# Performance work log

Measured on AMD Instinct MI355X. Metric: run time of the kernel, lower is better.

Reference implementation:

```python
import jax, jax.numpy as jnp
import numpy as np

B, T, C, H = 16, 2048, 1024, 64

def setup_inputs() -> dict:
    key = jax.random.key(0)
    kx, kq, kk, kv = jax.random.split(key, 4)
    x = jax.random.normal(kx, (B, T, C), dtype=jnp.float32)
    Wq = jax.random.normal(kq, (C, H), dtype=jnp.float32) * (C ** -0.5)
    Wk = jax.random.normal(kk, (C, H), dtype=jnp.float32) * (C ** -0.5)
    Wv = jax.random.normal(kv, (C, H), dtype=jnp.float32) * (C ** -0.5)
    return {"x": x, "Wq": Wq, "Wk": Wk, "Wv": Wv}

def reference(x, Wq, Wk, Wv):
    # q,k,v: [B,T,H]
    q = jnp.einsum('btc,ch->bth', x, Wq)
    k = jnp.einsum('btc,ch->bth', x, Wk)
    v = jnp.einsum('btc,ch->bth', x, Wv)
    scale = k.shape[-1] ** -0.5
    # scores: [B,T,T], causal mask then softmax (dropout=0 -> identity)
    w = jnp.einsum('bth,bsh->bts', q, k) * scale
    causal = jnp.tril(jnp.ones((x.shape[1], x.shape[1]), dtype=bool))
    w = jnp.where(causal[None, :, :], w, -jnp.inf)
    w = jax.nn.softmax(w, axis=-1)
    out = jnp.einsum('bts,bsh->bth', w, v)
    return out
```

## Files before the change

### kernel.cpp

```cpp
#include <hip/hip_runtime.h>


#define B_ 16
#define T_ 2048
#define C_ 1024
#define H_ 64
#define QK_ELEMS (B_ * T_ * H_)

typedef float  f32x4  __attribute__((ext_vector_type(4)));
typedef __bf16 bf16x8 __attribute__((ext_vector_type(8)));
typedef __bf16 bf16x4 __attribute__((ext_vector_type(4)));

__device__ __forceinline__ void glds16(const void* g, void* l) {
    __builtin_amdgcn_global_load_lds(
        (const __attribute__((address_space(1))) void*)g,
        (__attribute__((address_space(3))) void*)l, 16, 0, 0);
}

__global__ __launch_bounds__(256) void wt_kernel(const float* __restrict__ Wq,
                                                 const float* __restrict__ Wk,
                                                 const float* __restrict__ Wv,
                                                 __bf16* __restrict__ Wt) {
    __shared__ float tl[64][65];
    const int mat = blockIdx.x >> 4;
    const int c0  = (blockIdx.x & 15) * 64;
    const float* W = (mat == 0) ? Wq : (mat == 1) ? Wk : Wv;
    const int t  = threadIdx.x;
    const int r4 = t >> 6;
    const int cc = t & 63;
#pragma unroll
    for (int i = 0; i < 16; i++) {
        const int c = r4 + i * 4;
        tl[c][cc] = W[(size_t)(c0 + c) * H_ + cc];
    }
    __syncthreads();
#pragma unroll
    for (int i = 0; i < 16; i++) {
        const int h = r4 + i * 4;
        const int cc2 = ((((cc >> 3) ^ (h & 7)) << 3) | (cc & 7));
        Wt[(size_t)mat * 65536 + (size_t)h * C_ + c0 + cc2] = (__bf16)tl[cc][h];
    }
}

__global__ __launch_bounds__(256) void qkv_kernel(const float* __restrict__ x,
                                                  const __bf16* __restrict__ Wt,
                                                  __bf16* __restrict__ Qw,
                                                  __bf16* __restrict__ Kw,
                                                  __bf16* __restrict__ Vtw) {
    __shared__ __align__(16) __bf16 Alds[2][64 * 72];
    __shared__ __align__(16) __bf16 Blds[2][192 * 64];

    const int tid  = threadIdx.x;
    const int w    = tid >> 6;
    const int lane = tid & 63;
    const int quad = lane >> 4;
    const int l15  = lane & 15;
    const int wm   = (w & 1) * 32;
    const int wn   = (w >> 1) * 96;
    const int m0   = blockIdx.x * 64;

    f32x4 acc[12];
#pragma unroll
    for (int i = 0; i < 12; i++) acc[i] = (f32x4){0.f, 0.f, 0.f, 0.f};

    const int ar = tid >> 3;
    const int ac = (tid & 7) * 8;
    const float* xA = x + (size_t)(m0 + ar) * C_ + ac;
    const __bf16* bsrc = Wt + (size_t)(w * 48 + (lane >> 3)) * C_ + (lane & 7) * 8;

    float4 a0, a1, a2, a3;
    auto loadA = [&](int k0) {
        a0 = *(const float4*)(xA + k0);
        a1 = *(const float4*)(xA + k0 + 4);
        a2 = *(const float4*)(xA + k0 + 32 * C_);
        a3 = *(const float4*)(xA + k0 + 32 * C_ + 4);
    };
    auto storeA = [&](int buf) {
        bf16x8 v0, v1;
        v0[0]=(__bf16)a0.x; v0[1]=(__bf16)a0.y; v0[2]=(__bf16)a0.z; v0[3]=(__bf16)a0.w;
        v0[4]=(__bf16)a1.x; v0[5]=(__bf16)a1.y; v0[6]=(__bf16)a1.z; v0[7]=(__bf16)a1.w;
        v1[0]=(__bf16)a2.x; v1[1]=(__bf16)a2.y; v1[2]=(__bf16)a2.z; v1[3]=(__bf16)a2.w;
        v1[4]=(__bf16)a3.x; v1[5]=(__bf16)a3.y; v1[6]=(__bf16)a3.z; v1[7]=(__bf16)a3.w;
        *(bf16x8*)&Alds[buf][ar * 72 + ac]        = v0;
        *(bf16x8*)&Alds[buf][(ar + 32) * 72 + ac] = v1;
    };
    auto asyncB = [&](int k0, int buf) {
        __bf16* dst = &Blds[buf][(w * 48) * 64];
        const __bf16* src = bsrc + k0;
#pragma unroll
        for (int i = 0; i < 6; i++)
            glds16(src + (size_t)i * 8 * C_, dst + i * 8 * 64);
    };

    asyncB(0, 0); loadA(0); storeA(0);

    for (int k = 0; k < 16; k++) {
        __syncthreads();
        const int kn = k + 1;
        if (kn < 16) { asyncB(kn * 64, kn & 1); loadA(kn * 64); }
        const int buf = k & 1;
#pragma unroll
        for (int kh = 0; kh < 2; kh++) {
            bf16x8 af0 = *(const bf16x8*)&Alds[buf][(wm + l15) * 72 + kh * 32 + quad * 8];
            bf16x8 af1 = *(const bf16x8*)&Alds[buf][(wm + 16 + l15) * 72 + kh * 32 + quad * 8];
            const int ch8 = ((((kh << 2) + quad) ^ (l15 & 7)) << 3);
#pragma unroll
            for (int nt = 0; nt < 6; nt++) {
                bf16x8 bfr = *(const bf16x8*)&Blds[buf][(wn + nt * 16 + l15) * 64 + ch8];
                acc[nt]     = __builtin_amdgcn_mfma_f32_16x16x32_bf16(af0, bfr, acc[nt], 0, 0, 0);
                acc[6 + nt] = __builtin_amdgcn_mfma_f32_16x16x32_bf16(af1, bfr, acc[6 + nt], 0, 0, 0);
            }
        }
        if (kn < 16) storeA(kn & 1);
    }

#pragma unroll
    for (int mt = 0; mt < 2; mt++) {
        const int row0 = m0 + wm + mt * 16 + quad * 4;
#pragma unroll
        for (int nt = 0; nt < 6; nt++) {
            const int col = wn + nt * 16 + l15;
            const f32x4 a = acc[mt * 6 + nt];
            if (wn + nt * 16 < 64) {
#pragma unroll
                for (int r = 0; r < 4; r++)
                    Qw[(size_t)(row0 + r) * H_ + col] = (__bf16)a[r];
            } else if (wn + nt * 16 < 128) {
#pragma unroll
                for (int r = 0; r < 4; r++)
                    Kw[(size_t)(row0 + r) * H_ + col - 64] = (__bf16)a[r];
            }
        }
    }
    __bf16* Vt_l = &Alds[0][0];
    if (w >= 2) {
#pragma unroll
        for (int mt = 0; mt < 2; mt++) {
            const int t0 = wm + mt * 16 + quad * 4;
#pragma unroll
            for (int nt = 2; nt < 6; nt++) {
                const int h = (nt - 2) * 16 + l15;
                const f32x4 a = acc[mt * 6 + nt];
                bf16x4 pv;
                pv[0]=(__bf16)a[0]; pv[1]=(__bf16)a[1]; pv[2]=(__bf16)a[2]; pv[3]=(__bf16)a[3];
                *(bf16x4*)&Vt_l[h * 72 + t0] = pv;
            }
        }
    }
    __syncthreads();
    if (w >= 2) {
        const int bb   = m0 >> 11;
        const int tblk = m0 & 2047;
#pragma unroll
        for (int i = 0; i < 4; i++) {
            const int hh = (w - 2) * 32 + i * 8 + (lane >> 3);
            const int tt = (lane & 7) * 8;
            *(bf16x8*)(Vtw + (((size_t)(bb * H_ + hh)) << 11) + tblk + tt) =
                *(const bf16x8*)&Vt_l[hh * 72 + tt];
        }
    }
}

#define SCALE_LOG2E 0.18033688011112042f

__global__ __launch_bounds__(256) void attn_kernel(const __bf16* __restrict__ Qw,
                                                   const __bf16* __restrict__ Kw,
                                                   const __bf16* __restrict__ Vtw,
                                                   float* __restrict__ Opart,
                                                   float* __restrict__ Lpart) {
    __shared__ __align__(16) __bf16 Klds[2][64 * 72];
    __shared__ __align__(16) __bf16 Vlds[2][64 * 72];
    __shared__ __align__(16) __bf16 Plds[4][16 * 72];

    const int tid  = threadIdx.x;
    const int w    = tid >> 6;
    const int lane = tid & 63;
    const int quad = lane >> 4;
    const int l15  = lane & 15;

    const int b   = blockIdx.x & 15;
    const int cid = 79 - (blockIdx.x >> 4);
    int qi, ci;
    if (cid < 8)       { qi = cid;                  ci = 0; }
    else if (cid < 24) { qi = 8 + ((cid - 8) >> 1); ci = (cid - 8) & 1; }
    else if (cid < 48) { const int u = cid - 24; const int d = u / 3;
                         qi = 16 + d;               ci = u - d * 3; }
    else               { qi = 24 + ((cid - 48) >> 2); ci = (cid - 48) & 3; }
    const int j0 = ci * 8;
    const int j1 = (j0 + 8 < qi + 1) ? j0 + 8 : qi + 1;
    const int nj = j1 - j0;
    const int tq0 = qi * 64;
    const size_t bT = (size_t)b * T_;

    const __bf16* qp = Qw + (bT + tq0 + w * 16 + l15) * H_ + quad * 8;
    const bf16x8 qf0 = *(const bf16x8*)qp;
    const bf16x8 qf1 = *(const bf16x8*)(qp + 32);

    float l_acc = 0.f;
    f32x4 accO[4];
#pragma unroll
    for (int nt = 0; nt < 4; nt++) accO[nt] = (f32x4){0.f, 0.f, 0.f, 0.f};

    const int sr = tid >> 3;
    const int sc = (tid & 7) * 8;
    const __bf16* Kbase = Kw + (bT + sr) * H_ + sc;
    const __bf16* Vbase = Vtw + (((size_t)(b * H_ + sr)) << 11) + sc;

    bf16x8 kr0, kr1, vr0, vr1;
    auto loadTile = [&](int ts0) {
        kr0 = *(const bf16x8*)(Kbase + (size_t)ts0 * H_);
        kr1 = *(const bf16x8*)(Kbase + (size_t)(ts0 + 32) * H_);
        vr0 = *(const bf16x8*)(Vbase + ts0);
        vr1 = *(const bf16x8*)(Vbase + ts0 + ((size_t)32 << 11));
    };
    auto storeTile = [&](int buf) {
        *(bf16x8*)&Klds[buf][sr * 72 + sc]        = kr0;
        *(bf16x8*)&Klds[buf][(sr + 32) * 72 + sc] = kr1;
        *(bf16x8*)&Vlds[buf][sr * 72 + sc]        = vr0;
        *(bf16x8*)&Vlds[buf][(sr + 32) * 72 + sc] = vr1;
    };

    loadTile(j0 * 64); storeTile(0);

    for (int jj = 0; jj < nj; jj++) {
        const int j = j0 + jj;
        __syncthreads();
        if (jj + 1 < nj) loadTile((j + 1) * 64);
        const int buf = jj & 1;

        f32x4 s[4];
#pragma unroll
        for (int nt = 0; nt < 4; nt++) {
            const __bf16* kb = &Klds[buf][(nt * 16 + l15) * 72];
            bf16x8 kf0 = *(const bf16x8*)(kb + quad * 8);
            bf16x8 kf1 = *(const bf16x8*)(kb + 32 + quad * 8);
            f32x4 z = (f32x4){0.f, 0.f, 0.f, 0.f};
            z     = __builtin_amdgcn_mfma_f32_16x16x32_bf16(kf0, qf0, z, 0, 0, 0);
            s[nt] = __builtin_amdgcn_mfma_f32_16x16x32_bf16(kf1, qf1, z, 0, 0, 0);
        }

        float p[4][4];
        if (j == qi) {
            const int ts0 = j * 64;
            const int qg  = tq0 + w * 16 + l15;
#pragma unroll
            for (int nt = 0; nt < 4; nt++)
#pragma unroll
                for (int r = 0; r < 4; r++) {
                    const int key = ts0 + nt * 16 + quad * 4 + r;
                    float e = exp2f(__builtin_fmaf(s[nt][r], SCALE_LOG2E, -8.0f));
                    e = (key > qg) ? 0.f : e;
                    p[nt][r] = e;
                    l_acc += e;
                }
        } else {
#pragma unroll
            for (int nt = 0; nt < 4; nt++)
#pragma unroll
                for (int r = 0; r < 4; r++) {
                    float e = exp2f(__builtin_fmaf(s[nt][r], SCALE_LOG2E, -8.0f));
                    p[nt][r] = e;
                    l_acc += e;
                }
        }

        __bf16* pw = &Plds[w][l15 * 72 + quad * 4];
#pragma unroll
        for (int nt = 0; nt < 4; nt++) {
            bf16x4 pv;
            pv[0]=(__bf16)p[nt][0]; pv[1]=(__bf16)p[nt][1];
            pv[2]=(__bf16)p[nt][2]; pv[3]=(__bf16)p[nt][3];
            *(bf16x4*)(pw + nt * 16) = pv;
        }
        __asm__ __volatile__("s_waitcnt lgkmcnt(0)" ::: "memory");

        const __bf16* pr = &Plds[w][l15 * 72];
        bf16x8 pf0 = *(const bf16x8*)(pr + quad * 8);
        bf16x8 pf1 = *(const bf16x8*)(pr + 32 + quad * 8);
#pragma unroll
        for (int nt = 0; nt < 4; nt++) {
            const __bf16* vb = &Vlds[buf][(nt * 16 + l15) * 72];
            bf16x8 vf0 = *(const bf16x8*)(vb + quad * 8);
            bf16x8 vf1 = *(const bf16x8*)(vb + 32 + quad * 8);
            accO[nt] = __builtin_amdgcn_mfma_f32_16x16x32_bf16(pf0, vf0, accO[nt], 0, 0, 0);
            accO[nt] = __builtin_amdgcn_mfma_f32_16x16x32_bf16(pf1, vf1, accO[nt], 0, 0, 0);
        }
        if (jj + 1 < nj) storeTile((jj + 1) & 1);
    }

    l_acc += __shfl_xor(l_acc, 16);
    l_acc += __shfl_xor(l_acc, 32);

    const int slot = (((b << 5) + qi) << 2) + ci;
    float* Op = Opart + (size_t)slot * 4096;
#pragma unroll
    for (int nt = 0; nt < 4; nt++)
#pragma unroll
        for (int r = 0; r < 4; r++)
            Op[(w * 16 + quad * 4 + r) * 64 + nt * 16 + l15] = accO[nt][r];
    if (quad == 0) Lpart[slot * 64 + w * 16 + l15] = l_acc;
}

__global__ __launch_bounds__(256) void reduce_kernel(const float* __restrict__ Opart,
                                                     const float* __restrict__ Lpart,
                                                     float* __restrict__ out) {
    const int b  = blockIdx.x & 15;
    const int qi = blockIdx.x >> 4;
    const int nc = (qi >> 3) + 1;
    const int tid = threadIdx.x;
    const int q  = tid >> 2;
    const int hc = (tid & 3) * 16;
    const int sbase = ((b << 5) + qi) << 2;

    f32x4 s[4];
#pragma unroll
    for (int i = 0; i < 4; i++) s[i] = (f32x4){0.f, 0.f, 0.f, 0.f};
    float l = 0.f;
    for (int ci = 0; ci < nc; ci++) {
        const float* Op = Opart + (size_t)(sbase + ci) * 4096 + q * 64 + hc;
#pragma unroll
        for (int i = 0; i < 4; i++) s[i] += *(const f32x4*)(Op + i * 4);
        l += Lpart[(sbase + ci) * 64 + q];
    }
    const float inv = 1.f / l;
    float* o = out + ((size_t)b * T_ + qi * 64 + q) * H_ + hc;
#pragma unroll
    for (int i = 0; i < 4; i++) {
        f32x4 r = s[i] * inv;
        *(f32x4*)(o + i * 4) = r;
    }
}

extern "C" void kernel_launch(void* const* d_in, const int* in_sizes, int n_in,
                              void* d_out, int out_size, void* d_ws, size_t ws_size,
                              hipStream_t stream) {
    const float* x  = (const float*)d_in[0];
    const float* Wq = (const float*)d_in[1];
    const float* Wk = (const float*)d_in[2];
    const float* Wv = (const float*)d_in[3];
    float* out = (float*)d_out;

    __bf16* Qw  = (__bf16*)d_ws;
    __bf16* Kw  = Qw + QK_ELEMS;
    __bf16* Vtw = Kw + QK_ELEMS;
    __bf16* Wt  = Vtw + QK_ELEMS;
    float* Opart = (float*)((char*)d_ws + 16777216);
    float* Lpart = Opart + (size_t)2048 * 4096;

    wt_kernel<<<dim3(48), dim3(256), 0, stream>>>(Wq, Wk, Wv, Wt);
    qkv_kernel<<<dim3((B_ * T_) / 64), dim3(256), 0, stream>>>(x, Wt, Qw, Kw, Vtw);
    attn_kernel<<<dim3(1280), dim3(256), 0, stream>>>(Qw, Kw, Vtw, Opart, Lpart);
    reduce_kernel<<<dim3(512), dim3(256), 0, stream>>>(Opart, Lpart, out);
}
```

Measured before the change: 244.2 us.

## Process two query tiles per attention block and stage K/V via async LDS loads

The attention kernel now handles a pair of adjacent 64-row query tiles per block, so every K/V tile staged in LDS feeds two query tiles. This halves the grid and the K/V global traffic per query. K and V now go straight into LDS through global_load_lds with an XOR swizzle that the QKV kernel writes into K and V^T, replacing the register-staged padded copies. The QKV projection also prefetches x two steps ahead. The costs are more registers from two accumulator sets, a changed split-to-chunk mapping in the reduce, and possible load imbalance.

```diff
diff --git a/kernel.cpp b/kernel.cpp
--- a/kernel.cpp
+++ b/kernel.cpp
@@ -68,19 +68,23 @@
     const float* xA = x + (size_t)(m0 + ar) * C_ + ac;
     const __bf16* bsrc = Wt + (size_t)(w * 48 + (lane >> 3)) * C_ + (lane & 7) * 8;
 
-    float4 a0, a1, a2, a3;
-    auto loadA = [&](int k0) {
-        a0 = *(const float4*)(xA + k0);
-        a1 = *(const float4*)(xA + k0 + 4);
-        a2 = *(const float4*)(xA + k0 + 32 * C_);
-        a3 = *(const float4*)(xA + k0 + 32 * C_ + 4);
+    float4 a[2][4];
+    auto loadA = [&](int slot, int k0) {
+        a[slot][0] = *(const float4*)(xA + k0);
+        a[slot][1] = *(const float4*)(xA + k0 + 4);
+        a[slot][2] = *(const float4*)(xA + k0 + 32 * C_);
+        a[slot][3] = *(const float4*)(xA + k0 + 32 * C_ + 4);
     };
-    auto storeA = [&](int buf) {
+    auto storeA = [&](int slot, int buf) {
         bf16x8 v0, v1;
-        v0[0]=(__bf16)a0.x; v0[1]=(__bf16)a0.y; v0[2]=(__bf16)a0.z; v0[3]=(__bf16)a0.w;
-        v0[4]=(__bf16)a1.x; v0[5]=(__bf16)a1.y; v0[6]=(__bf16)a1.z; v0[7]=(__bf16)a1.w;
-        v1[0]=(__bf16)a2.x; v1[1]=(__bf16)a2.y; v1[2]=(__bf16)a2.z; v1[3]=(__bf16)a2.w;
-        v1[4]=(__bf16)a3.x; v1[5]=(__bf16)a3.y; v1[6]=(__bf16)a3.z; v1[7]=(__bf16)a3.w;
+        v0[0]=(__bf16)a[slot][0].x; v0[1]=(__bf16)a[slot][0].y;
+        v0[2]=(__bf16)a[slot][0].z; v0[3]=(__bf16)a[slot][0].w;
+        v0[4]=(__bf16)a[slot][1].x; v0[5]=(__bf16)a[slot][1].y;
+        v0[6]=(__bf16)a[slot][1].z; v0[7]=(__bf16)a[slot][1].w;
+        v1[0]=(__bf16)a[slot][2].x; v1[1]=(__bf16)a[slot][2].y;
+        v1[2]=(__bf16)a[slot][2].z; v1[3]=(__bf16)a[slot][2].w;
+        v1[4]=(__bf16)a[slot][3].x; v1[5]=(__bf16)a[slot][3].y;
+        v1[6]=(__bf16)a[slot][3].z; v1[7]=(__bf16)a[slot][3].w;
         *(bf16x8*)&Alds[buf][ar * 72 + ac]        = v0;
         *(bf16x8*)&Alds[buf][(ar + 32) * 72 + ac] = v1;
     };
@@ -92,12 +96,15 @@
             glds16(src + (size_t)i * 8 * C_, dst + i * 8 * 64);
     };
 
-    asyncB(0, 0); loadA(0); storeA(0);
+    loadA(0, 0); loadA(1, 64);
+    asyncB(0, 0);
+    storeA(0, 0);
 
     for (int k = 0; k < 16; k++) {
         __syncthreads();
         const int kn = k + 1;
-        if (kn < 16) { asyncB(kn * 64, kn & 1); loadA(kn * 64); }
+        if (kn < 16) asyncB(kn * 64, kn & 1);
+        if (k + 2 < 16) loadA(k & 1, (k + 2) * 64);
         const int buf = k & 1;
 #pragma unroll
         for (int kh = 0; kh < 2; kh++) {
@@ -111,7 +118,7 @@
                 acc[6 + nt] = __builtin_amdgcn_mfma_f32_16x16x32_bf16(af1, bfr, acc[6 + nt], 0, 0, 0);
             }
         }
-        if (kn < 16) storeA(kn & 1);
+        if (kn < 16) storeA(kn & 1, kn & 1);
     }
 
 #pragma unroll
@@ -120,15 +127,19 @@
 #pragma unroll
         for (int nt = 0; nt < 6; nt++) {
             const int col = wn + nt * 16 + l15;
-            const f32x4 a = acc[mt * 6 + nt];
+            const f32x4 acv = acc[mt * 6 + nt];
             if (wn + nt * 16 < 64) {
 #pragma unroll
                 for (int r = 0; r < 4; r++)
-                    Qw[(size_t)(row0 + r) * H_ + col] = (__bf16)a[r];
+                    Qw[(size_t)(row0 + r) * H_ + col] = (__bf16)acv[r];
             } else if (wn + nt * 16 < 128) {
-#pragma unroll
-                for (int r = 0; r < 4; r++)
-                    Kw[(size_t)(row0 + r) * H_ + col - 64] = (__bf16)a[r];
+                const int h = col - 64;
+#pragma unroll
+                for (int r = 0; r < 4; r++) {
+                    const int row = row0 + r;
+                    const int hs  = (((h >> 3) ^ (row & 7)) << 3) | (h & 7);
+                    Kw[(size_t)row * H_ + hs] = (__bf16)acv[r];
+                }
             }
         }
     }
@@ -140,9 +151,10 @@
 #pragma unroll
             for (int nt = 2; nt < 6; nt++) {
                 const int h = (nt - 2) * 16 + l15;
-                const f32x4 a = acc[mt * 6 + nt];
+                const f32x4 acv = acc[mt * 6 + nt];
                 bf16x4 pv;
-                pv[0]=(__bf16)a[0]; pv[1]=(__bf16)a[1]; pv[2]=(__bf16)a[2]; pv[3]=(__bf16)a[3];
+                pv[0]=(__bf16)acv[0]; pv[1]=(__bf16)acv[1];
+                pv[2]=(__bf16)acv[2]; pv[3]=(__bf16)acv[3];
                 *(bf16x4*)&Vt_l[h * 72 + t0] = pv;
             }
         }
@@ -154,9 +166,9 @@
 #pragma unroll
         for (int i = 0; i < 4; i++) {
             const int hh = (w - 2) * 32 + i * 8 + (lane >> 3);
-            const int tt = (lane & 7) * 8;
-            *(bf16x8*)(Vtw + (((size_t)(bb * H_ + hh)) << 11) + tblk + tt) =
-                *(const bf16x8*)&Vt_l[hh * 72 + tt];
+            const int cs = (((lane & 7) ^ (lane >> 3)) << 3);
+            *(bf16x8*)(Vtw + (((size_t)(bb * H_ + hh)) << 11) + tblk + ((lane & 7) << 3)) =
+                *(const bf16x8*)&Vt_l[hh * 72 + cs];
         }
     }
 }
@@ -168,9 +180,9 @@
                                                    const __bf16* __restrict__ Vtw,
                                                    float* __restrict__ Opart,
                                                    float* __restrict__ Lpart) {
-    __shared__ __align__(16) __bf16 Klds[2][64 * 72];
-    __shared__ __align__(16) __bf16 Vlds[2][64 * 72];
-    __shared__ __align__(16) __bf16 Plds[4][16 * 72];
+    __shared__ __align__(16) __bf16 Klds[2][64 * 64];
+    __shared__ __align__(16) __bf16 Vlds[2][64 * 64];
+    __shared__ __align__(16) __bf16 Plds[2][4][16 * 72];
 
     const int tid  = threadIdx.x;
     const int w    = tid >> 6;
@@ -179,126 +191,139 @@
     const int l15  = lane & 15;
 
     const int b   = blockIdx.x & 15;
-    const int cid = 79 - (blockIdx.x >> 4);
-    int qi, ci;
-    if (cid < 8)       { qi = cid;                  ci = 0; }
-    else if (cid < 24) { qi = 8 + ((cid - 8) >> 1); ci = (cid - 8) & 1; }
-    else if (cid < 48) { const int u = cid - 24; const int d = u / 3;
-                         qi = 16 + d;               ci = u - d * 3; }
-    else               { qi = 24 + ((cid - 48) >> 2); ci = (cid - 48) & 3; }
+    const int cid = blockIdx.x >> 4;
+    int i, ci;
+    if (cid < 16)      { i = 15 - (cid >> 2); ci = cid & 3; }
+    else if (cid < 28) { const int u = cid - 16; i = 11 - u / 3; ci = u % 3; }
+    else if (cid < 36) { const int u = cid - 28; i = 7 - (u >> 1); ci = u & 1; }
+    else               { i = 3 - (cid - 36); ci = 0; }
+
+    const int jmax = 2 * i + 1;
     const int j0 = ci * 8;
-    const int j1 = (j0 + 8 < qi + 1) ? j0 + 8 : qi + 1;
+    const int j1 = (j0 + 8 < jmax + 1) ? j0 + 8 : jmax + 1;
     const int nj = j1 - j0;
-    const int tq0 = qi * 64;
+    const int qA0 = 2 * i * 64;
     const size_t bT = (size_t)b * T_;
 
-    const __bf16* qp = Qw + (bT + tq0 + w * 16 + l15) * H_ + quad * 8;
-    const bf16x8 qf0 = *(const bf16x8*)qp;
-    const bf16x8 qf1 = *(const bf16x8*)(qp + 32);
-
-    float l_acc = 0.f;
-    f32x4 accO[4];
-#pragma unroll
-    for (int nt = 0; nt < 4; nt++) accO[nt] = (f32x4){0.f, 0.f, 0.f, 0.f};
-
-    const int sr = tid >> 3;
-    const int sc = (tid & 7) * 8;
-    const __bf16* Kbase = Kw + (bT + sr) * H_ + sc;
-    const __bf16* Vbase = Vtw + (((size_t)(b * H_ + sr)) << 11) + sc;
-
-    bf16x8 kr0, kr1, vr0, vr1;
-    auto loadTile = [&](int ts0) {
-        kr0 = *(const bf16x8*)(Kbase + (size_t)ts0 * H_);
-        kr1 = *(const bf16x8*)(Kbase + (size_t)(ts0 + 32) * H_);
-        vr0 = *(const bf16x8*)(Vbase + ts0);
-        vr1 = *(const bf16x8*)(Vbase + ts0 + ((size_t)32 << 11));
+    const __bf16* qpA = Qw + (bT + qA0 + w * 16 + l15) * H_ + quad * 8;
+    const bf16x8 qfA0 = *(const bf16x8*)qpA;
+    const bf16x8 qfA1 = *(const bf16x8*)(qpA + 32);
+    const bf16x8 qfB0 = *(const bf16x8*)(qpA + 64 * H_);
+    const bf16x8 qfB1 = *(const bf16x8*)(qpA + 64 * H_ + 32);
+
+    float lA = 0.f, lB = 0.f;
+    f32x4 accA[4], accB[4];
+#pragma unroll
+    for (int nt = 0; nt < 4; nt++) {
+        accA[nt] = (f32x4){0.f, 0.f, 0.f, 0.f};
+        accB[nt] = (f32x4){0.f, 0.f, 0.f, 0.f};
+    }
+
+    auto stage = [&](int ts0, int buf) {
+        const __bf16* Ks = Kw + (bT + ts0) * H_;
+        const __bf16* Vs = Vtw + (((size_t)(b * H_)) << 11) + ts0;
+#pragma unroll
+        for (int c = 0; c < 2; c++) {
+            const int g   = w * 2 + c;
+            const int row = g * 8 + (lane >> 3);
+            const int cb  = (lane & 7) * 8;
+            glds16(Ks + (size_t)row * H_ + cb, &Klds[buf][g * 512]);
+            glds16(Vs + ((size_t)row << 11) + cb, &Vlds[buf][g * 512]);
+        }
     };
-    auto storeTile = [&](int buf) {
-        *(bf16x8*)&Klds[buf][sr * 72 + sc]        = kr0;
-        *(bf16x8*)&Klds[buf][(sr + 32) * 72 + sc] = kr1;
-        *(bf16x8*)&Vlds[buf][sr * 72 + sc]        = vr0;
-        *(bf16x8*)&Vlds[buf][(sr + 32) * 72 + sc] = vr1;
-    };
-
-    loadTile(j0 * 64); storeTile(0);
+
+    stage(j0 * 64, 0);
 
     for (int jj = 0; jj < nj; jj++) {
         const int j = j0 + jj;
         __syncthreads();
-        if (jj + 1 < nj) loadTile((j + 1) * 64);
+        if (jj + 1 < nj) stage((j + 1) * 64, (jj + 1) & 1);
         const int buf = jj & 1;
-
-        f32x4 s[4];
+        const bool doA = (j <= 2 * i);
+        const int ts0 = j * 64;
+        const int qgA = qA0 + w * 16 + l15;
+
 #pragma unroll
         for (int nt = 0; nt < 4; nt++) {
-            const __bf16* kb = &Klds[buf][(nt * 16 + l15) * 72];
-            bf16x8 kf0 = *(const bf16x8*)(kb + quad * 8);
-            bf16x8 kf1 = *(const bf16x8*)(kb + 32 + quad * 8);
-            f32x4 z = (f32x4){0.f, 0.f, 0.f, 0.f};
-            z     = __builtin_amdgcn_mfma_f32_16x16x32_bf16(kf0, qf0, z, 0, 0, 0);
-            s[nt] = __builtin_amdgcn_mfma_f32_16x16x32_bf16(kf1, qf1, z, 0, 0, 0);
-        }
-
-        float p[4][4];
-        if (j == qi) {
-            const int ts0 = j * 64;
-            const int qg  = tq0 + w * 16 + l15;
-#pragma unroll
-            for (int nt = 0; nt < 4; nt++)
+            const __bf16* kb = &Klds[buf][(nt * 16 + l15) * 64];
+            bf16x8 kf0 = *(const bf16x8*)(kb + ((quad ^ (l15 & 7)) << 3));
+            bf16x8 kf1 = *(const bf16x8*)(kb + (((4 + quad) ^ (l15 & 7)) << 3));
+            const int key0 = ts0 + nt * 16 + quad * 4;
+
+            if (doA) {
+                f32x4 z = (f32x4){0.f, 0.f, 0.f, 0.f};
+                z = __builtin_amdgcn_mfma_f32_16x16x32_bf16(kf0, qfA0, z, 0, 0, 0);
+                z = __builtin_amdgcn_mfma_f32_16x16x32_bf16(kf1, qfA1, z, 0, 0, 0);
+                bf16x4 pv;
 #pragma unroll
                 for (int r = 0; r < 4; r++) {
-                    const int key = ts0 + nt * 16 + quad * 4 + r;
-                    float e = exp2f(__builtin_fmaf(s[nt][r], SCALE_LOG2E, -8.0f));
-                    e = (key > qg) ? 0.f : e;
-                    p[nt][r] = e;
-                    l_acc += e;
+                    float e = exp2f(__builtin_fmaf(z[r], SCALE_LOG2E, -8.0f));
+                    if (j == 2 * i && key0 + r > qgA) e = 0.f;
+                    pv[r] = (__bf16)e;
+                    lA += e;
                 }
-        } else {
-#pragma unroll
-            for (int nt = 0; nt < 4; nt++)
+                *(bf16x4*)&Plds[0][w][l15 * 72 + nt * 16 + quad * 4] = pv;
+            }
+            {
+                f32x4 z = (f32x4){0.f, 0.f, 0.f, 0.f};
+                z = __builtin_amdgcn_mfma_f32_16x16x32_bf16(kf0, qfB0, z, 0, 0, 0);
+                z = __builtin_amdgcn_mfma_f32_16x16x32_bf16(kf1, qfB1, z, 0, 0, 0);
+                bf16x4 pv;
 #pragma unroll
                 for (int r = 0; r < 4; r++) {
-                    float e = exp2f(__builtin_fmaf(s[nt][r], SCALE_LOG2E, -8.0f));
-                    p[nt][r] = e;
-                    l_acc += e;
+                    float e = exp2f(__builtin_fmaf(z[r], SCALE_LOG2E, -8.0f));
+                    if (j == jmax && key0 + r > qgA + 64) e = 0.f;
+                    pv[r] = (__bf16)e;
+                    lB += e;
                 }
-        }
-
-        __bf16* pw = &Plds[w][l15 * 72 + quad * 4];
+                *(bf16x4*)&Plds[1][w][l15 * 72 + nt * 16 + quad * 4] = pv;
+            }
+        }
+        __asm__ __volatile__("s_waitcnt lgkmcnt(0)" ::: "memory");
+
+        const __bf16* prA = &Plds[0][w][l15 * 72];
+        const __bf16* prB = &Plds[1][w][l15 * 72];
+        bf16x8 pfA0, pfA1;
+        if (doA) {
+            pfA0 = *(const bf16x8*)(prA + quad * 8);
+            pfA1 = *(const bf16x8*)(prA + 32 + quad * 8);
+        }
+        bf16x8 pfB0 = *(const bf16x8*)(prB + quad * 8);
+        bf16x8 pfB1 = *(const bf16x8*)(prB + 32 + quad * 8);
 #pragma unroll
         for (int nt = 0; nt < 4; nt++) {
-            bf16x4 pv;
-            pv[0]=(__bf16)p[nt][0]; pv[1]=(__bf16)p[nt][1];
-            pv[2]=(__bf16)p[nt][2]; pv[3]=(__bf16)p[nt][3];
-            *(bf16x4*)(pw + nt * 16) = pv;
-        }
-        __asm__ __volatile__("s_waitcnt lgkmcnt(0)" ::: "memory");
-
-        const __bf16* pr = &Plds[w][l15 * 72];
-        bf16x8 pf0 = *(const bf16x8*)(pr + quad * 8);
-        bf16x8 pf1 = *(const bf16x8*)(pr + 32 + quad * 8);
-#pragma unroll
-        for (int nt = 0; nt < 4; nt++) {
-            const __bf16* vb = &Vlds[buf][(nt * 16 + l15) * 72];
-            bf16x8 vf0 = *(const bf16x8*)(vb + quad * 8);
-            bf16x8 vf1 = *(const bf16x8*)(vb + 32 + quad * 8);
-            accO[nt] = __builtin_amdgcn_mfma_f32_16x16x32_bf16(pf0, vf0, accO[nt], 0, 0, 0);
-            accO[nt] = __builtin_amdgcn_mfma_f32_16x16x32_bf16(pf1, vf1, accO[nt], 0, 0, 0);
-        }
-        if (jj + 1 < nj) storeTile((jj + 1) & 1);
-    }
-
-    l_acc += __shfl_xor(l_acc, 16);
-    l_acc += __shfl_xor(l_acc, 32);
-
-    const int slot = (((b << 5) + qi) << 2) + ci;
-    float* Op = Opart + (size_t)slot * 4096;
+            const __bf16* vb = &Vlds[buf][(nt * 16 + l15) * 64];
+            bf16x8 vf0 = *(const bf16x8*)(vb + ((quad ^ (l15 & 7)) << 3));
+            bf16x8 vf1 = *(const bf16x8*)(vb + (((4 + quad) ^ (l15 & 7)) << 3));
+            if (doA) {
+                accA[nt] = __builtin_amdgcn_mfma_f32_16x16x32_bf16(pfA0, vf0, accA[nt], 0, 0, 0);
+                accA[nt] = __builtin_amdgcn_mfma_f32_16x16x32_bf16(pfA1, vf1, accA[nt], 0, 0, 0);
+            }
+            accB[nt] = __builtin_amdgcn_mfma_f32_16x16x32_bf16(pfB0, vf0, accB[nt], 0, 0, 0);
+            accB[nt] = __builtin_amdgcn_mfma_f32_16x16x32_bf16(pfB1, vf1, accB[nt], 0, 0, 0);
+        }
+    }
+
+    lA += __shfl_xor(lA, 16); lA += __shfl_xor(lA, 32);
+    lB += __shfl_xor(lB, 16); lB += __shfl_xor(lB, 32);
+
+    const int qiA = 2 * i;
+    const int slotA = ((((b << 5) + qiA) << 2) + ci);
+    const int slotB = ((((b << 5) + qiA + 1) << 2) + ci);
+    float* OpA = Opart + (size_t)slotA * 4096;
+    float* OpB = Opart + (size_t)slotB * 4096;
 #pragma unroll
     for (int nt = 0; nt < 4; nt++)
 #pragma unroll
-        for (int r = 0; r < 4; r++)
-            Op[(w * 16 + quad * 4 + r) * 64 + nt * 16 + l15] = accO[nt][r];
-    if (quad == 0) Lpart[slot * 64 + w * 16 + l15] = l_acc;
+        for (int r = 0; r < 4; r++) {
+            const int o = (w * 16 + quad * 4 + r) * 64 + nt * 16 + l15;
+            OpA[o] = accA[nt][r];
+            OpB[o] = accB[nt][r];
+        }
+    if (quad == 0) {
+        Lpart[slotA * 64 + w * 16 + l15] = lA;
+        Lpart[slotB * 64 + w * 16 + l15] = lB;
+    }
 }
 
 __global__ __launch_bounds__(256) void reduce_kernel(const float* __restrict__ Opart,
@@ -306,7 +331,7 @@
                                                      float* __restrict__ out) {
     const int b  = blockIdx.x & 15;
     const int qi = blockIdx.x >> 4;
-    const int nc = (qi >> 3) + 1;
+    const int nc = ((qi & ~1) + 9) >> 3;
     const int tid = threadIdx.x;
     const int q  = tid >> 2;
     const int hc = (tid & 3) * 16;
@@ -349,6 +374,6 @@
 
     wt_kernel<<<dim3(48), dim3(256), 0, stream>>>(Wq, Wk, Wv, Wt);
     qkv_kernel<<<dim3((B_ * T_) / 64), dim3(256), 0, stream>>>(x, Wt, Qw, Kw, Vtw);
-    attn_kernel<<<dim3(1280), dim3(256), 0, stream>>>(Qw, Kw, Vtw, Opart, Lpart);
+    attn_kernel<<<dim3(640), dim3(256), 0, stream>>>(Qw, Kw, Vtw, Opart, Lpart);
     reduce_kernel<<<dim3(512), dim3(256), 0, stream>>>(Opart, Lpart, out);
 }
```

New measurement: 242.6 us. Within noise of the previous version (-0.6%).
